# Performance work log

Measured on AMD Instinct MI355X. Metric: run time of the kernel, lower is better.

The kernel has to match this reference:

```python
import math
import jax, jax.numpy as jnp
import numpy as np

B, N, D, E = 4, 256, 256, 128  # batch, nodes, node_dim, edge_dim


def setup_inputs() -> dict:
    key = jax.random.key(0)
    ks = jax.random.split(key, 12)
    s_d = 1.0 / math.sqrt(D)
    s_e = 1.0 / math.sqrt(E)
    s_3d = 1.0 / math.sqrt(3 * D)
    return {
        "h": jax.random.normal(ks[0], (B, N, D), jnp.float32),
        "g": jax.random.normal(ks[1], (B, N, N, E), jnp.float32),
        "node_mask": jnp.ones((B, N), dtype=bool),
        # attention projections (stored as (in, out); x @ W == torch Linear)
        "Wq": jax.random.normal(ks[2], (D, D), jnp.float32) * s_d,
        "Wk": jax.random.normal(ks[3], (E, D), jnp.float32) * s_e,
        "Wv": jax.random.normal(ks[4], (E, D), jnp.float32) * s_e,
        # edge_to_node MLP: Linear(D,D) -> SiLU -> Linear(D,D)
        "W1a": jax.random.normal(ks[5], (D, D), jnp.float32) * s_d,
        "b1a": jnp.zeros((D,), jnp.float32),
        "W2a": jax.random.normal(ks[6], (D, D), jnp.float32) * s_d,
        "b2a": jnp.zeros((D,), jnp.float32),
        # node_to_edge MLP: Linear(3D,E) -> SiLU -> Linear(E,E)
        "W1b": jax.random.normal(ks[7], (3 * D, E), jnp.float32) * s_3d,
        "b1b": jnp.zeros((E,), jnp.float32),
        "W2b": jax.random.normal(ks[8], (E, E), jnp.float32) * s_e,
        "b2b": jnp.zeros((E,), jnp.float32),
    }


def reference(h, g, node_mask, Wq, Wk, Wv, W1a, b1a, W2a, b2a, W1b, b1b, W2b, b2b):
    scale = 1.0 / math.sqrt(D)
    # Edge-to-Node attention
    q = h @ Wq                                   # (B,N,D)
    k = jnp.einsum('bije,ed->bijd', g, Wk)       # (B,N,N,D)
    v = jnp.einsum('bije,ed->bijd', g, Wv)       # (B,N,N,D)
    scores = jnp.einsum('bid,bijd->bij', q, k) * scale
    edge_mask = node_mask[:, :, None] & node_mask[:, None, :]
    scores = jnp.where(edge_mask, scores, -10000.0)
    alpha = jax.nn.softmax(scores, axis=2)
    alpha = alpha * node_mask[:, :, None].astype(alpha.dtype)
    node_agg = jnp.einsum('bij,bijd->bid', alpha, v)
    # edge_to_node MLP (dropout = identity at inference)
    h_update = h + (jax.nn.silu(node_agg @ W1a + b1a) @ W2a + b2a)
    # Node-to-Edge: split W1b so the (B,N,N,3D) concat is never materialized;
    # pair @ W1b == h_i @ Wi + h_j @ Wj + (h_i*h_j) @ Wh  (mathematically identical)
    Wi, Wj, Wh = W1b[:D], W1b[D:2 * D], W1b[2 * D:]
    xi = (h_update @ Wi)[:, :, None, :]          # (B,N,1,E)
    xj = (h_update @ Wj)[:, None, :, :]          # (B,1,N,E)
    had = h_update[:, :, None, :] * h_update[:, None, :, :]  # (B,N,N,D)
    pre = xi + xj + jnp.einsum('bijd,de->bije', had, Wh) + b1b
    g_update = g + (jax.nn.silu(pre) @ W2b + b2b)
    return (h_update, g_update)
```

## Files before the change

kernel.cpp:

```cpp
#include <hip/hip_runtime.h>

typedef unsigned short u16;
typedef short short8 __attribute__((ext_vector_type(8)));
typedef float f32x4 __attribute__((ext_vector_type(4)));

#define DEV __device__ __forceinline__

DEV float bf2f(u16 u) { return __uint_as_float(((unsigned int)u) << 16); }
DEV u16 f2bf(float f) {
    unsigned int u = __float_as_uint(f);
    u += 0x7fffu + ((u >> 16) & 1u);
    return (u16)(u >> 16);
}
DEV float sigf(float x) { return 1.0f / (1.0f + __expf(-x)); }

__global__ __launch_bounds__(256) void k_prep_t(const float* __restrict__ W1b,
                                                const float* __restrict__ W2b,
                                                u16* __restrict__ WhT,
                                                u16* __restrict__ WjT,
                                                u16* __restrict__ W2bT) {
    __shared__ u16 sT[64 * 72];
    int t = threadIdx.x, blk = blockIdx.x;
    const float* src;
    u16* dst;
    int R, C, ri, ci;
    if (blk < 16) {
        int m = blk >> 3;
        src = W1b + (m ? 256 * 128 : 512 * 128);
        dst = m ? WjT : WhT;
        R = 256; C = 128;
        int lb = blk & 7;
        ri = lb >> 1; ci = lb & 1;
    } else {
        src = W2b; dst = W2bT; R = 128; C = 128;
        int lb = blk - 16;
        ri = lb >> 1; ci = lb & 1;
    }
    int lr = t >> 2, q = t & 3;
#pragma unroll
    for (int s4 = 0; s4 < 4; ++s4) {
        float4 v = *(const float4*)(src + (size_t)(ri * 64 + lr) * C + ci * 64 + q * 16 + s4 * 4);
        int c0 = q * 16 + s4 * 4;
        sT[(c0 + 0) * 72 + lr] = f2bf(v.x);
        sT[(c0 + 1) * 72 + lr] = f2bf(v.y);
        sT[(c0 + 2) * 72 + lr] = f2bf(v.z);
        sT[(c0 + 3) * 72 + lr] = f2bf(v.w);
    }
    __syncthreads();
    int dr = t >> 2;
#pragma unroll
    for (int s8 = 0; s8 < 2; ++s8) {
        int cc = q * 16 + s8 * 8;
        ushort4 w0, w1;
        w0.x = sT[dr * 72 + cc + 0]; w0.y = sT[dr * 72 + cc + 1];
        w0.z = sT[dr * 72 + cc + 2]; w0.w = sT[dr * 72 + cc + 3];
        w1.x = sT[dr * 72 + cc + 4]; w1.y = sT[dr * 72 + cc + 5];
        w1.z = sT[dr * 72 + cc + 6]; w1.w = sT[dr * 72 + cc + 7];
        *(ushort4*)(dst + (size_t)(ci * 64 + dr) * R + ri * 64 + cc) = w0;
        *(ushort4*)(dst + (size_t)(ci * 64 + dr) * R + ri * 64 + cc + 4) = w1;
    }
}

__global__ __launch_bounds__(128) void k_prep_m1(const float* __restrict__ Wq,
                                                 const float* __restrict__ Wk,
                                                 float* __restrict__ M1) {
    __shared__ float swq[256];
    int t = threadIdx.x, c = blockIdx.x;
    swq[t] = Wq[c * 256 + t];
    swq[t + 128] = Wq[c * 256 + t + 128];
    __syncthreads();
    const float* wk = Wk + (size_t)t * 256;
    float acc = 0.f;
#pragma unroll 4
    for (int d = 0; d < 256; d += 4) {
        float4 b = *(const float4*)(wk + d);
        acc += swq[d] * b.x + swq[d + 1] * b.y + swq[d + 2] * b.z + swq[d + 3] * b.w;
    }
    M1[c * 128 + t] = acc;
}

__global__ __launch_bounds__(128) void k_qk(const float* __restrict__ h,
                                            const float* __restrict__ M1,
                                            float* __restrict__ qk) {
    __shared__ float sh[256];
    int t = threadIdx.x, bi = blockIdx.x;
    sh[t] = h[(size_t)bi * 256 + t];
    sh[t + 128] = h[(size_t)bi * 256 + t + 128];
    __syncthreads();
    float acc = 0.f;
#pragma unroll 8
    for (int c = 0; c < 256; ++c) acc += sh[c] * M1[c * 128 + t];
    qk[bi * 128 + t] = acc;
}

__global__ __launch_bounds__(256) void k_attn(const float* __restrict__ g,
                                              const float* __restrict__ qk,
                                              float* __restrict__ gagg) {
    __shared__ __align__(16) u16 sg[32768];
    __shared__ float sqk[128];
    __shared__ float ssc[256];
    __shared__ float sred[4];
    __shared__ float sacc[512];
    int t = threadIdx.x, bi = blockIdx.x;
    int lane = t & 63, wv = t >> 6;
    if (t < 128) sqk[t] = qk[bi * 128 + t] * 0.0625f;
    const float* gb = g + (size_t)bi * 32768;
#pragma unroll
    for (int it = 0; it < 32; ++it) {
        int idx = (it * 256 + t) * 4;
        float4 v = *(const float4*)(gb + idx);
        ushort4 pk;
        pk.x = f2bf(v.x); pk.y = f2bf(v.y); pk.z = f2bf(v.z); pk.w = f2bf(v.w);
        *(ushort4*)(sg + idx) = pk;
    }
    __syncthreads();

    float s = 0.f;
#pragma unroll 8
    for (int it = 0; it < 64; ++it) {
        int p2 = (it + t) & 63;
        unsigned int u = *(const unsigned int*)(sg + t * 128 + 2 * p2);
        float2 qv = *(const float2*)(sqk + 2 * p2);
        s += bf2f((u16)(u & 0xffffu)) * qv.x + bf2f((u16)(u >> 16)) * qv.y;
    }

    float v = s;
#pragma unroll
    for (int off = 32; off > 0; off >>= 1) v = fmaxf(v, __shfl_xor(v, off));
    if (lane == 0) sred[wv] = v;
    __syncthreads();
    float m = fmaxf(fmaxf(sred[0], sred[1]), fmaxf(sred[2], sred[3]));
    float pv = __expf(s - m);
    ssc[t] = pv;
    float sv = pv;
#pragma unroll
    for (int off = 32; off > 0; off >>= 1) sv += __shfl_xor(sv, off);
    __syncthreads();
    if (lane == 0) sred[wv] = sv;
    __syncthreads();
    float s_sum = sred[0] + sred[1] + sred[2] + sred[3];

    int epair = t & 63, jq = t >> 6;
    float a0 = 0.f, a1 = 0.f;
    const u16* sq = sg + jq * 8192 + 2 * epair;
#pragma unroll 8
    for (int jj = 0; jj < 64; ++jj) {
        unsigned int u = *(const unsigned int*)(sq + jj * 128);
        float p = ssc[jq * 64 + jj];
        a0 += p * bf2f((u16)(u & 0xffffu));
        a1 += p * bf2f((u16)(u >> 16));
    }
    sacc[jq * 128 + 2 * epair] = a0;
    sacc[jq * 128 + 2 * epair + 1] = a1;
    __syncthreads();
    if (t < 128)
        gagg[bi * 128 + t] = (sacc[t] + sacc[128 + t] + sacc[256 + t] + sacc[384 + t]) / s_sum;
}

__global__ __launch_bounds__(256) void k_hmlp(
    const float* __restrict__ h, const float* __restrict__ gagg,
    const float* __restrict__ Wv, const float* __restrict__ W1a,
    const float* __restrict__ b1a, const float* __restrict__ W2a,
    const float* __restrict__ b2a, const float* __restrict__ W1b,
    const float* __restrict__ b1b,
    float* __restrict__ hu_ws, float* __restrict__ xi_ws, float* __restrict__ out) {
    __shared__ float sgg[128];
    __shared__ float sna[256];
    __shared__ float su[256];
    __shared__ float shu[256];
    int t = threadIdx.x, bi = blockIdx.x;
    if (t < 128) sgg[t] = gagg[bi * 128 + t];
    __syncthreads();
    float na = 0.f;
#pragma unroll 4
    for (int e2 = 0; e2 < 128; ++e2) na += sgg[e2] * Wv[(size_t)e2 * 256 + t];
    sna[t] = na;
    __syncthreads();
    float u1 = b1a[t];
#pragma unroll 4
    for (int c = 0; c < 256; ++c) u1 += sna[c] * W1a[(size_t)c * 256 + t];
    float uu = u1 * sigf(u1);
    su[t] = uu;
    __syncthreads();
    float hv = h[(size_t)bi * 256 + t] + b2a[t];
#pragma unroll 4
    for (int c = 0; c < 256; ++c) hv += su[c] * W2a[(size_t)c * 256 + t];
    shu[t] = hv;
    hu_ws[(size_t)bi * 256 + t] = hv;
    out[(size_t)bi * 256 + t] = hv;
    __syncthreads();
    if (t < 128) {
        float x = b1b[t];
#pragma unroll 4
        for (int c = 0; c < 256; ++c) x += shu[c] * W1b[(size_t)c * 128 + t];
        xi_ws[bi * 128 + t] = x;
    }
}

__global__ __launch_bounds__(256, 4) void k_gupd(
    const float* __restrict__ g, const float* __restrict__ hu_ws,
    const float* __restrict__ xi_ws,
    const u16* __restrict__ WhT, const u16* __restrict__ WjT,
    const u16* __restrict__ W2bT, const float* __restrict__ b2b,
    float* __restrict__ out) {
    __shared__ __align__(16) char uni[36864];
    __shared__ float s_hui[256];
    __shared__ float s_xi[128];
    u16* sA = (u16*)uni;
    u16* sB = (u16*)(uni + 18432);
    u16* sP = (u16*)uni;
    float* sF = (float*)uni;

    int t = threadIdx.x;
    int bi = blockIdx.x;
    int jb = blockIdx.y;
    int b = bi >> 8;
    int j0 = jb * 128;
    int w = t >> 6, lane = t & 63;
    int n = lane & 15, quad = lane >> 4;

    s_hui[t] = hu_ws[(size_t)bi * 256 + t];
    if (t < 128) s_xi[t] = xi_ws[bi * 128 + t];
    __syncthreads();

    f32x4 acc[2][8];
#pragma unroll
    for (int et = 0; et < 8; ++et) {
        float xiv = s_xi[et * 16 + n];
        f32x4 iv = {xiv, xiv, xiv, xiv};
        acc[0][et] = iv;
        acc[1][et] = iv;
    }

    const float* huj = hu_ws + (size_t)(b * 256 + j0) * 256;
    int r2 = t >> 2, q = t & 3;
    for (int kc = 0; kc < 4; ++kc) {
        int d0 = kc * 64;
#pragma unroll
        for (int half = 0; half < 2; ++half) {
            int row = r2 + half * 64;
            const float* src = huj + (size_t)row * 256 + d0 + q * 16;
#pragma unroll
            for (int s4 = 0; s4 < 4; ++s4) {
                float4 v = *(const float4*)(src + s4 * 4);
                ushort4 pk;
                pk.x = f2bf(v.x); pk.y = f2bf(v.y); pk.z = f2bf(v.z); pk.w = f2bf(v.w);
                *(ushort4*)(sA + row * 72 + q * 16 + s4 * 4) = pk;
            }
        }
#pragma unroll
        for (int half = 0; half < 2; ++half) {
            int e = r2 + half * 64;
            const u16* wh = WhT + (size_t)e * 256 + d0 + q * 16;
            const u16* wj = WjT + (size_t)e * 256 + d0 + q * 16;
            u16* dstp = sB + e * 72 + q * 16;
            const float* hp = s_hui + d0 + q * 16;
#pragma unroll
            for (int s8 = 0; s8 < 2; ++s8) {
                ushort4 ha = *(const ushort4*)(wh + s8 * 8);
                ushort4 hb = *(const ushort4*)(wh + s8 * 8 + 4);
                ushort4 ja = *(const ushort4*)(wj + s8 * 8);
                ushort4 jb4 = *(const ushort4*)(wj + s8 * 8 + 4);
                const float* hh = hp + s8 * 8;
                ushort4 oa, ob;
                oa.x = f2bf(hh[0] * bf2f(ha.x) + bf2f(ja.x));
                oa.y = f2bf(hh[1] * bf2f(ha.y) + bf2f(ja.y));
                oa.z = f2bf(hh[2] * bf2f(ha.z) + bf2f(ja.z));
                oa.w = f2bf(hh[3] * bf2f(ha.w) + bf2f(ja.w));
                ob.x = f2bf(hh[4] * bf2f(hb.x) + bf2f(jb4.x));
                ob.y = f2bf(hh[5] * bf2f(hb.y) + bf2f(jb4.y));
                ob.z = f2bf(hh[6] * bf2f(hb.z) + bf2f(jb4.z));
                ob.w = f2bf(hh[7] * bf2f(hb.w) + bf2f(jb4.w));
                *(ushort4*)(dstp + s8 * 8) = oa;
                *(ushort4*)(dstp + s8 * 8 + 4) = ob;
            }
        }
        __syncthreads();
#pragma unroll
        for (int s = 0; s < 2; ++s) {
            int kk = s * 32;
            short8 af0 = *(const short8*)(sA + (w * 32 + n) * 72 + kk + quad * 8);
            short8 af1 = *(const short8*)(sA + (w * 32 + 16 + n) * 72 + kk + quad * 8);
#pragma unroll
            for (int et = 0; et < 8; ++et) {
                short8 bfr = *(const short8*)(sB + (et * 16 + n) * 72 + kk + quad * 8);
                acc[0][et] = __builtin_amdgcn_mfma_f32_16x16x32_bf16(af0, bfr, acc[0][et], 0, 0, 0);
                acc[1][et] = __builtin_amdgcn_mfma_f32_16x16x32_bf16(af1, bfr, acc[1][et], 0, 0, 0);
            }
        }
        __syncthreads();
    }

#pragma unroll
    for (int mti = 0; mti < 2; ++mti)
#pragma unroll
        for (int et = 0; et < 8; ++et)
#pragma unroll
            for (int r = 0; r < 4; ++r) {
                float x = acc[mti][et][r];
                sP[(w * 32 + mti * 16 + quad * 4 + r) * 136 + et * 16 + n] = f2bf(x * sigf(x));
            }
    __syncthreads();

#pragma unroll
    for (int et = 0; et < 8; ++et) {
        float bv = b2b[et * 16 + n];
        f32x4 iv = {bv, bv, bv, bv};
        acc[0][et] = iv;
        acc[1][et] = iv;
    }
#pragma unroll
    for (int ks = 0; ks < 4; ++ks) {
        int f0 = ks * 32;
        short8 a0 = *(const short8*)(sP + (w * 32 + n) * 136 + f0 + quad * 8);
        short8 a1 = *(const short8*)(sP + (w * 32 + 16 + n) * 136 + f0 + quad * 8);
#pragma unroll
        for (int et = 0; et < 8; ++et) {
            short8 bfr = *(const short8*)(W2bT + (et * 16 + n) * 128 + f0 + quad * 8);
            acc[0][et] = __builtin_amdgcn_mfma_f32_16x16x32_bf16(a0, bfr, acc[0][et], 0, 0, 0);
            acc[1][et] = __builtin_amdgcn_mfma_f32_16x16x32_bf16(a1, bfr, acc[1][et], 0, 0, 0);
        }
    }

    const float* gbase = g + ((size_t)bi * 256 + j0) * 128;
    float* obase = out + 262144 + ((size_t)bi * 256 + j0) * 128;
#pragma unroll
    for (int mti = 0; mti < 2; ++mti) {
        __syncthreads();
#pragma unroll
        for (int et = 0; et < 8; ++et)
#pragma unroll
            for (int r = 0; r < 4; ++r)
                sF[(w * 16 + quad * 4 + r) * 132 + et * 16 + n] = acc[mti][et][r];
        __syncthreads();
#pragma unroll
        for (int it = 0; it < 8; ++it) {
            int fidx = it * 256 + t;
            int rp = fidx >> 5;
            int c4 = fidx & 31;
            int jrow = (rp >> 4) * 32 + mti * 16 + (rp & 15);
            float4 gv = *(const float4*)(gbase + (size_t)jrow * 128 + c4 * 4);
            float4 pv2 = *(const float4*)(sF + rp * 132 + c4 * 4);
            float4 ov;
            ov.x = gv.x + pv2.x; ov.y = gv.y + pv2.y;
            ov.z = gv.z + pv2.z; ov.w = gv.w + pv2.w;
            *(float4*)(obase + (size_t)jrow * 128 + c4 * 4) = ov;
        }
    }
}

extern "C" void kernel_launch(void* const* d_in, const int* in_sizes, int n_in,
                              void* d_out, int out_size, void* d_ws, size_t ws_size,
                              hipStream_t stream) {
    const float* h   = (const float*)d_in[0];
    const float* g   = (const float*)d_in[1];
    const float* Wq  = (const float*)d_in[3];
    const float* Wk  = (const float*)d_in[4];
    const float* Wv  = (const float*)d_in[5];
    const float* W1a = (const float*)d_in[6];
    const float* b1a = (const float*)d_in[7];
    const float* W2a = (const float*)d_in[8];
    const float* b2a = (const float*)d_in[9];
    const float* W1b = (const float*)d_in[10];
    const float* b1b = (const float*)d_in[11];
    const float* W2b = (const float*)d_in[12];
    const float* b2b = (const float*)d_in[13];

    float* ws   = (float*)d_ws;
    float* M1   = ws;
    float* qk   = M1 + 32768;
    float* gagg = qk + 131072;
    float* hu   = gagg + 131072;
    float* xi   = hu + 262144;
    u16* WhT    = (u16*)(xi + 131072);
    u16* WjT    = WhT + 32768;
    u16* W2bT   = WjT + 32768;

    float* out = (float*)d_out;

    k_prep_t<<<20, 256, 0, stream>>>(W1b, W2b, WhT, WjT, W2bT);
    k_prep_m1<<<256, 128, 0, stream>>>(Wq, Wk, M1);
    k_qk<<<1024, 128, 0, stream>>>(h, M1, qk);
    k_attn<<<1024, 256, 0, stream>>>(g, qk, gagg);
    k_hmlp<<<1024, 256, 0, stream>>>(h, gagg, Wv, W1a, b1a, W2a, b2a, W1b, b1b,
                                     hu, xi, out);
    k_gupd<<<dim3(1024, 2), 256, 0, stream>>>(g, hu, xi, WhT, WjT, W2bT, b2b, out);
}
```

Baseline: 452.2 us.

## Restructure edge update: precompute xj and bf16 h_update, fold Wv into W1a

The edge-update kernel no longer stages h_j and a per-row scaled weight matrix through shared memory. It reads precomputed bf16 h_update rows, forms the Hadamard products in registers as MFMA A fragments, and uses the unscaled Wh as the B operand. The xj term is computed once per node in the MLP kernel rather than through Wj in every tile. Wv·W1a is folded into one precomputed matrix, the qk and MLP kernels handle two rows per block, and the final residual add writes directly from registers without a shared-memory transpose. Costs: uncoalesced global loads and stores in the epilogue, B fragments read from global memory, and an extra bf16 rounding of h_update.

```diff
diff --git a/kernel.cpp b/kernel.cpp
--- a/kernel.cpp
+++ b/kernel.cpp
@@ -12,28 +12,30 @@
     u += 0x7fffu + ((u >> 16) & 1u);
     return (u16)(u >> 16);
 }
+DEV unsigned cvtpk_bf16(float lo, float hi) {
+    unsigned r;
+    asm("v_cvt_pk_bf16_f32 %0, %1, %2" : "=v"(r) : "v"(lo), "v"(hi));
+    return r;
+}
 DEV float sigf(float x) { return 1.0f / (1.0f + __expf(-x)); }
 
 __global__ __launch_bounds__(256) void k_prep_t(const float* __restrict__ W1b,
                                                 const float* __restrict__ W2b,
                                                 u16* __restrict__ WhT,
-                                                u16* __restrict__ WjT,
                                                 u16* __restrict__ W2bT) {
     __shared__ u16 sT[64 * 72];
     int t = threadIdx.x, blk = blockIdx.x;
     const float* src;
     u16* dst;
     int R, C, ri, ci;
-    if (blk < 16) {
-        int m = blk >> 3;
-        src = W1b + (m ? 256 * 128 : 512 * 128);
-        dst = m ? WjT : WhT;
+    if (blk < 8) {
+        src = W1b + 512 * 128;
+        dst = WhT;
         R = 256; C = 128;
-        int lb = blk & 7;
-        ri = lb >> 1; ci = lb & 1;
+        ri = blk >> 1; ci = blk & 1;
     } else {
         src = W2b; dst = W2bT; R = 128; C = 128;
-        int lb = blk - 16;
+        int lb = blk - 8;
         ri = lb >> 1; ci = lb & 1;
     }
     int lr = t >> 2, q = t & 3;
@@ -79,18 +81,45 @@
     M1[c * 128 + t] = acc;
 }
 
-__global__ __launch_bounds__(128) void k_qk(const float* __restrict__ h,
+__global__ __launch_bounds__(256) void k_prep_m2(const float* __restrict__ Wv,
+                                                 const float* __restrict__ W1a,
+                                                 float* __restrict__ M2) {
+    __shared__ float sv[256];
+    int t = threadIdx.x, e = blockIdx.x;
+    sv[t] = Wv[(size_t)e * 256 + t];
+    __syncthreads();
+    float acc = 0.f;
+#pragma unroll 16
+    for (int d = 0; d < 256; ++d) acc += sv[d] * W1a[d * 256 + t];
+    M2[e * 256 + t] = acc;
+}
+
+__global__ __launch_bounds__(256) void k_qk(const float* __restrict__ h,
                                             const float* __restrict__ M1,
                                             float* __restrict__ qk) {
-    __shared__ float sh[256];
-    int t = threadIdx.x, bi = blockIdx.x;
-    sh[t] = h[(size_t)bi * 256 + t];
-    sh[t + 128] = h[(size_t)bi * 256 + t + 128];
-    __syncthreads();
-    float acc = 0.f;
-#pragma unroll 8
-    for (int c = 0; c < 256; ++c) acc += sh[c] * M1[c * 128 + t];
-    qk[bi * 128 + t] = acc;
+    __shared__ float sh[2][256];
+    __shared__ float sp[2][2][128];
+    int t = threadIdx.x;
+    int r0 = blockIdx.x * 2;
+    sh[0][t] = h[(size_t)r0 * 256 + t];
+    sh[1][t] = h[(size_t)(r0 + 1) * 256 + t];
+    __syncthreads();
+    int e = t & 127, ch = t >> 7;
+    float a0 = 0.f, a1 = 0.f;
+    const float* m1 = M1 + (size_t)ch * 128 * 128;
+    const float* s0 = &sh[0][ch * 128];
+    const float* s1 = &sh[1][ch * 128];
+#pragma unroll 16
+    for (int c = 0; c < 128; ++c) {
+        float m = m1[c * 128 + e];
+        a0 += s0[c] * m;
+        a1 += s1[c] * m;
+    }
+    sp[ch][0][e] = a0;
+    sp[ch][1][e] = a1;
+    __syncthreads();
+    if (t < 128) qk[(size_t)r0 * 128 + t] = sp[0][0][t] + sp[1][0][t];
+    else qk[(size_t)(r0 + 1) * 128 + (t - 128)] = sp[0][1][t - 128] + sp[1][1][t - 128];
 }
 
 __global__ __launch_bounds__(256) void k_attn(const float* __restrict__ g,
@@ -159,136 +188,125 @@
 
 __global__ __launch_bounds__(256) void k_hmlp(
     const float* __restrict__ h, const float* __restrict__ gagg,
-    const float* __restrict__ Wv, const float* __restrict__ W1a,
-    const float* __restrict__ b1a, const float* __restrict__ W2a,
-    const float* __restrict__ b2a, const float* __restrict__ W1b,
-    const float* __restrict__ b1b,
-    float* __restrict__ hu_ws, float* __restrict__ xi_ws, float* __restrict__ out) {
-    __shared__ float sgg[128];
-    __shared__ float sna[256];
-    __shared__ float su[256];
-    __shared__ float shu[256];
-    int t = threadIdx.x, bi = blockIdx.x;
-    if (t < 128) sgg[t] = gagg[bi * 128 + t];
-    __syncthreads();
-    float na = 0.f;
-#pragma unroll 4
-    for (int e2 = 0; e2 < 128; ++e2) na += sgg[e2] * Wv[(size_t)e2 * 256 + t];
-    sna[t] = na;
-    __syncthreads();
-    float u1 = b1a[t];
-#pragma unroll 4
-    for (int c = 0; c < 256; ++c) u1 += sna[c] * W1a[(size_t)c * 256 + t];
-    float uu = u1 * sigf(u1);
-    su[t] = uu;
-    __syncthreads();
-    float hv = h[(size_t)bi * 256 + t] + b2a[t];
-#pragma unroll 4
-    for (int c = 0; c < 256; ++c) hv += su[c] * W2a[(size_t)c * 256 + t];
-    shu[t] = hv;
-    hu_ws[(size_t)bi * 256 + t] = hv;
-    out[(size_t)bi * 256 + t] = hv;
-    __syncthreads();
-    if (t < 128) {
-        float x = b1b[t];
-#pragma unroll 4
-        for (int c = 0; c < 256; ++c) x += shu[c] * W1b[(size_t)c * 128 + t];
-        xi_ws[bi * 128 + t] = x;
-    }
+    const float* __restrict__ M2, const float* __restrict__ b1a,
+    const float* __restrict__ W2a, const float* __restrict__ b2a,
+    const float* __restrict__ W1b, const float* __restrict__ b1b,
+    float* __restrict__ hu_ws, u16* __restrict__ hub_ws,
+    float* __restrict__ xi_ws, float* __restrict__ xj_ws,
+    float* __restrict__ out) {
+    __shared__ float sgg[2][128];
+    __shared__ float su[2][256];
+    __shared__ float shu[2][256];
+    int t = threadIdx.x;
+    int r0 = blockIdx.x * 2;
+    sgg[t >> 7][t & 127] = gagg[(size_t)(r0 + (t >> 7)) * 128 + (t & 127)];
+    __syncthreads();
+    float a0 = b1a[t], a1 = a0;
+#pragma unroll 16
+    for (int e = 0; e < 128; ++e) {
+        float mm = M2[e * 256 + t];
+        a0 += sgg[0][e] * mm;
+        a1 += sgg[1][e] * mm;
+    }
+    su[0][t] = a0 * sigf(a0);
+    su[1][t] = a1 * sigf(a1);
+    __syncthreads();
+    float b2av = b2a[t];
+    float h0 = h[(size_t)r0 * 256 + t] + b2av;
+    float h1 = h[(size_t)(r0 + 1) * 256 + t] + b2av;
+#pragma unroll 16
+    for (int c = 0; c < 256; ++c) {
+        float mm = W2a[c * 256 + t];
+        h0 += su[0][c] * mm;
+        h1 += su[1][c] * mm;
+    }
+    shu[0][t] = h0;
+    shu[1][t] = h1;
+    hu_ws[(size_t)r0 * 256 + t] = h0;
+    hu_ws[(size_t)(r0 + 1) * 256 + t] = h1;
+    hub_ws[(size_t)r0 * 256 + t] = f2bf(h0);
+    hub_ws[(size_t)(r0 + 1) * 256 + t] = f2bf(h1);
+    out[(size_t)r0 * 256 + t] = h0;
+    out[(size_t)(r0 + 1) * 256 + t] = h1;
+    __syncthreads();
+    int e = t & 127, which = t >> 7;
+    const float* Wp = W1b + (size_t)which * 32768;
+    float x0 = which ? 0.f : b1b[e];
+    float x1 = x0;
+#pragma unroll 16
+    for (int c = 0; c < 256; ++c) {
+        float mm = Wp[c * 128 + e];
+        x0 += shu[0][c] * mm;
+        x1 += shu[1][c] * mm;
+    }
+    float* dst = which ? xj_ws : xi_ws;
+    dst[(size_t)r0 * 128 + e] = x0;
+    dst[(size_t)(r0 + 1) * 128 + e] = x1;
 }
 
 __global__ __launch_bounds__(256, 4) void k_gupd(
     const float* __restrict__ g, const float* __restrict__ hu_ws,
-    const float* __restrict__ xi_ws,
-    const u16* __restrict__ WhT, const u16* __restrict__ WjT,
-    const u16* __restrict__ W2bT, const float* __restrict__ b2b,
-    float* __restrict__ out) {
-    __shared__ __align__(16) char uni[36864];
+    const u16* __restrict__ hub_ws,
+    const float* __restrict__ xi_ws, const float* __restrict__ xj_ws,
+    const u16* __restrict__ WhT, const u16* __restrict__ W2bT,
+    const float* __restrict__ b2b, float* __restrict__ out) {
+    __shared__ __align__(16) u16 sP[128 * 136];
     __shared__ float s_hui[256];
     __shared__ float s_xi[128];
-    u16* sA = (u16*)uni;
-    u16* sB = (u16*)(uni + 18432);
-    u16* sP = (u16*)uni;
-    float* sF = (float*)uni;
 
     int t = threadIdx.x;
     int bi = blockIdx.x;
     int jb = blockIdx.y;
     int b = bi >> 8;
     int j0 = jb * 128;
-    int w = t >> 6, lane = t & 63;
-    int n = lane & 15, quad = lane >> 4;
+    int w = t >> 6, lane = t & 63, n = lane & 15, quad = lane >> 4;
 
     s_hui[t] = hu_ws[(size_t)bi * 256 + t];
-    if (t < 128) s_xi[t] = xi_ws[bi * 128 + t];
-    __syncthreads();
-
+    if (t < 128) s_xi[t] = xi_ws[(size_t)bi * 128 + t];
+    __syncthreads();
+
+    int jr = w * 32 + quad * 4;
+
+    const float* xjp = xj_ws + (size_t)(b * 256 + j0) * 128;
     f32x4 acc[2][8];
 #pragma unroll
-    for (int et = 0; et < 8; ++et) {
-        float xiv = s_xi[et * 16 + n];
-        f32x4 iv = {xiv, xiv, xiv, xiv};
-        acc[0][et] = iv;
-        acc[1][et] = iv;
-    }
-
-    const float* huj = hu_ws + (size_t)(b * 256 + j0) * 256;
-    int r2 = t >> 2, q = t & 3;
+    for (int mti = 0; mti < 2; ++mti)
+#pragma unroll
+        for (int et = 0; et < 8; ++et) {
+            int e = et * 16 + n;
+            float xiv = s_xi[e];
+#pragma unroll
+            for (int r = 0; r < 4; ++r)
+                acc[mti][et][r] = xiv + xjp[(size_t)(jr + mti * 16 + r) * 128 + e];
+        }
+
+    const u16* hub = hub_ws + (size_t)(b * 256 + j0) * 256;
+    int row0 = w * 32 + n;
+#pragma unroll
     for (int kc = 0; kc < 4; ++kc) {
-        int d0 = kc * 64;
-#pragma unroll
-        for (int half = 0; half < 2; ++half) {
-            int row = r2 + half * 64;
-            const float* src = huj + (size_t)row * 256 + d0 + q * 16;
-#pragma unroll
-            for (int s4 = 0; s4 < 4; ++s4) {
-                float4 v = *(const float4*)(src + s4 * 4);
-                ushort4 pk;
-                pk.x = f2bf(v.x); pk.y = f2bf(v.y); pk.z = f2bf(v.z); pk.w = f2bf(v.w);
-                *(ushort4*)(sA + row * 72 + q * 16 + s4 * 4) = pk;
+#pragma unroll
+        for (int s = 0; s < 2; ++s) {
+            int c0 = kc * 64 + s * 32 + quad * 8;
+            short8 hj0 = *(const short8*)(hub + (size_t)row0 * 256 + c0);
+            short8 hj1 = *(const short8*)(hub + (size_t)(row0 + 16) * 256 + c0);
+            float4 hA = *(const float4*)(s_hui + c0);
+            float4 hB = *(const float4*)(s_hui + c0 + 4);
+            float hi8[8] = {hA.x, hA.y, hA.z, hA.w, hB.x, hB.y, hB.z, hB.w};
+            union { short8 s8; unsigned u[4]; } a0v, a1v;
+#pragma unroll
+            for (int k = 0; k < 4; ++k) {
+                a0v.u[k] = cvtpk_bf16(bf2f((u16)hj0[2 * k]) * hi8[2 * k],
+                                      bf2f((u16)hj0[2 * k + 1]) * hi8[2 * k + 1]);
+                a1v.u[k] = cvtpk_bf16(bf2f((u16)hj1[2 * k]) * hi8[2 * k],
+                                      bf2f((u16)hj1[2 * k + 1]) * hi8[2 * k + 1]);
+            }
+#pragma unroll
+            for (int et = 0; et < 8; ++et) {
+                short8 bfr = *(const short8*)(WhT + (size_t)(et * 16 + n) * 256 + c0);
+                acc[0][et] = __builtin_amdgcn_mfma_f32_16x16x32_bf16(a0v.s8, bfr, acc[0][et], 0, 0, 0);
+                acc[1][et] = __builtin_amdgcn_mfma_f32_16x16x32_bf16(a1v.s8, bfr, acc[1][et], 0, 0, 0);
             }
         }
-#pragma unroll
-        for (int half = 0; half < 2; ++half) {
-            int e = r2 + half * 64;
-            const u16* wh = WhT + (size_t)e * 256 + d0 + q * 16;
-            const u16* wj = WjT + (size_t)e * 256 + d0 + q * 16;
-            u16* dstp = sB + e * 72 + q * 16;
-            const float* hp = s_hui + d0 + q * 16;
-#pragma unroll
-            for (int s8 = 0; s8 < 2; ++s8) {
-                ushort4 ha = *(const ushort4*)(wh + s8 * 8);
-                ushort4 hb = *(const ushort4*)(wh + s8 * 8 + 4);
-                ushort4 ja = *(const ushort4*)(wj + s8 * 8);
-                ushort4 jb4 = *(const ushort4*)(wj + s8 * 8 + 4);
-                const float* hh = hp + s8 * 8;
-                ushort4 oa, ob;
-                oa.x = f2bf(hh[0] * bf2f(ha.x) + bf2f(ja.x));
-                oa.y = f2bf(hh[1] * bf2f(ha.y) + bf2f(ja.y));
-                oa.z = f2bf(hh[2] * bf2f(ha.z) + bf2f(ja.z));
-                oa.w = f2bf(hh[3] * bf2f(ha.w) + bf2f(ja.w));
-                ob.x = f2bf(hh[4] * bf2f(hb.x) + bf2f(jb4.x));
-                ob.y = f2bf(hh[5] * bf2f(hb.y) + bf2f(jb4.y));
-                ob.z = f2bf(hh[6] * bf2f(hb.z) + bf2f(jb4.z));
-                ob.w = f2bf(hh[7] * bf2f(hb.w) + bf2f(jb4.w));
-                *(ushort4*)(dstp + s8 * 8) = oa;
-                *(ushort4*)(dstp + s8 * 8 + 4) = ob;
-            }
-        }
-        __syncthreads();
-#pragma unroll
-        for (int s = 0; s < 2; ++s) {
-            int kk = s * 32;
-            short8 af0 = *(const short8*)(sA + (w * 32 + n) * 72 + kk + quad * 8);
-            short8 af1 = *(const short8*)(sA + (w * 32 + 16 + n) * 72 + kk + quad * 8);
-#pragma unroll
-            for (int et = 0; et < 8; ++et) {
-                short8 bfr = *(const short8*)(sB + (et * 16 + n) * 72 + kk + quad * 8);
-                acc[0][et] = __builtin_amdgcn_mfma_f32_16x16x32_bf16(af0, bfr, acc[0][et], 0, 0, 0);
-                acc[1][et] = __builtin_amdgcn_mfma_f32_16x16x32_bf16(af1, bfr, acc[1][et], 0, 0, 0);
-            }
-        }
-        __syncthreads();
     }
 
 #pragma unroll
@@ -316,7 +334,7 @@
         short8 a1 = *(const short8*)(sP + (w * 32 + 16 + n) * 136 + f0 + quad * 8);
 #pragma unroll
         for (int et = 0; et < 8; ++et) {
-            short8 bfr = *(const short8*)(W2bT + (et * 16 + n) * 128 + f0 + quad * 8);
+            short8 bfr = *(const short8*)(W2bT + (size_t)(et * 16 + n) * 128 + f0 + quad * 8);
             acc[0][et] = __builtin_amdgcn_mfma_f32_16x16x32_bf16(a0, bfr, acc[0][et], 0, 0, 0);
             acc[1][et] = __builtin_amdgcn_mfma_f32_16x16x32_bf16(a1, bfr, acc[1][et], 0, 0, 0);
         }
@@ -326,26 +344,18 @@
     float* obase = out + 262144 + ((size_t)bi * 256 + j0) * 128;
 #pragma unroll
     for (int mti = 0; mti < 2; ++mti) {
-        __syncthreads();
+        float gv[32];
 #pragma unroll
         for (int et = 0; et < 8; ++et)
 #pragma unroll
             for (int r = 0; r < 4; ++r)
-                sF[(w * 16 + quad * 4 + r) * 132 + et * 16 + n] = acc[mti][et][r];
-        __syncthreads();
-#pragma unroll
-        for (int it = 0; it < 8; ++it) {
-            int fidx = it * 256 + t;
-            int rp = fidx >> 5;
-            int c4 = fidx & 31;
-            int jrow = (rp >> 4) * 32 + mti * 16 + (rp & 15);
-            float4 gv = *(const float4*)(gbase + (size_t)jrow * 128 + c4 * 4);
-            float4 pv2 = *(const float4*)(sF + rp * 132 + c4 * 4);
-            float4 ov;
-            ov.x = gv.x + pv2.x; ov.y = gv.y + pv2.y;
-            ov.z = gv.z + pv2.z; ov.w = gv.w + pv2.w;
-            *(float4*)(obase + (size_t)jrow * 128 + c4 * 4) = ov;
-        }
+                gv[et * 4 + r] = gbase[(size_t)(jr + mti * 16 + r) * 128 + et * 16 + n];
+#pragma unroll
+        for (int et = 0; et < 8; ++et)
+#pragma unroll
+            for (int r = 0; r < 4; ++r)
+                obase[(size_t)(jr + mti * 16 + r) * 128 + et * 16 + n] =
+                    gv[et * 4 + r] + acc[mti][et][r];
     }
 }
 
@@ -368,21 +378,24 @@
 
     float* ws   = (float*)d_ws;
     float* M1   = ws;
-    float* qk   = M1 + 32768;
+    float* M2   = M1 + 32768;
+    float* qk   = M2 + 32768;
+    float* xj   = qk;
     float* gagg = qk + 131072;
     float* hu   = gagg + 131072;
     float* xi   = hu + 262144;
-    u16* WhT    = (u16*)(xi + 131072);
-    u16* WjT    = WhT + 32768;
-    u16* W2bT   = WjT + 32768;
+    u16* hub    = (u16*)(xi + 131072);
+    u16* WhT    = hub + 262144;
+    u16* W2bT   = WhT + 32768;
 
     float* out = (float*)d_out;
 
-    k_prep_t<<<20, 256, 0, stream>>>(W1b, W2b, WhT, WjT, W2bT);
+    k_prep_t<<<12, 256, 0, stream>>>(W1b, W2b, WhT, W2bT);
     k_prep_m1<<<256, 128, 0, stream>>>(Wq, Wk, M1);
-    k_qk<<<1024, 128, 0, stream>>>(h, M1, qk);
+    k_prep_m2<<<128, 256, 0, stream>>>(Wv, W1a, M2);
+    k_qk<<<512, 256, 0, stream>>>(h, M1, qk);
     k_attn<<<1024, 256, 0, stream>>>(g, qk, gagg);
-    k_hmlp<<<1024, 256, 0, stream>>>(h, gagg, Wv, W1a, b1a, W2a, b2a, W1b, b1b,
-                                     hu, xi, out);
-    k_gupd<<<dim3(1024, 2), 256, 0, stream>>>(g, hu, xi, WhT, WjT, W2bT, b2b, out);
-}
+    k_hmlp<<<512, 256, 0, stream>>>(h, gagg, M2, b1a, W2a, b2a, W1b, b1b,
+                                    hu, hub, xi, xj, out);
+    k_gupd<<<dim3(1024, 2), 256, 0, stream>>>(g, hu, hub, xi, xj, WhT, W2bT, b2b, out);
+}
```

Result: no change. 454.0 us (+0.4%).
